# Optimization experiments

Measured on AMD Instinct MI355X. Metric: run time of the kernel, lower is better.

## Reference

```python
import jax, jax.numpy as jnp
import numpy as np


def setup_inputs() -> dict:
    key = jax.random.key(0)
    ks = jax.random.split(key, 5)
    b, n, d = 1, 768, 128
    scale = 1.0 / np.sqrt(d)
    x = jax.random.normal(ks[0], (b, n, d), dtype=jnp.float32)
    W_in = jax.random.normal(ks[1], (d, d), dtype=jnp.float32) * scale
    b_in = jax.random.normal(ks[2], (d,), dtype=jnp.float32) * 0.02
    W_out = jax.random.normal(ks[3], (d, d), dtype=jnp.float32) * scale
    b_out = jax.random.normal(ks[4], (d,), dtype=jnp.float32) * 0.02
    return {"x": x, "W_in": W_in, "b_in": b_in, "W_out": W_out, "b_out": b_out}


def reference(x, W_in, b_in, W_out, b_out):
    # proj_in applied to x (original calls it twice on the same input; identical result)
    left = jnp.einsum('bid,ed->bie', x, W_in) + b_in          # [b, n, d]
    # broadcast outer product: [b, i, 1, d] * [b, 1, j, d] -> [b, i, j, d]
    outer = left[:, :, None, :] * left[:, None, :, :]
    # proj_out over feature dim
    out = jnp.einsum('bijd,ed->bije', outer, W_out) + b_out    # [b, n, n, d]
    return out
```

## Files before the change

kernel.cpp:

```cpp
#include <hip/hip_runtime.h>

#define Nn 768
#define Dd 128
#define LDP 136

typedef __attribute__((ext_vector_type(8))) short bf16x8;
typedef __attribute__((ext_vector_type(4))) float f32x4;
typedef __attribute__((ext_vector_type(4))) int   i32x4;

static __device__ __forceinline__ unsigned short f2bf(float f) {
  unsigned int u = __builtin_bit_cast(unsigned int, f);
  u += 0x7fffu + ((u >> 16) & 1u);
  return (unsigned short)(u >> 16);
}
static __device__ __forceinline__ float bf2f(unsigned short h) {
  unsigned int u = ((unsigned int)h) << 16;
  return __builtin_bit_cast(float, u);
}
static __device__ __forceinline__ unsigned int cvtpk(float lo, float hi) {
  unsigned int r;
  asm("v_cvt_pk_bf16_f32 %0, %1, %2" : "=v"(r) : "v"(lo), "v"(hi));
  return r;
}

__global__ __launch_bounds__(128)
void k_left(const float* __restrict__ x, const float* __restrict__ Win,
            const float* __restrict__ bin, unsigned short* __restrict__ left) {
  __shared__ float sx[Dd];
  const int i = blockIdx.x;
  const int e = threadIdx.x;
  sx[e] = x[i * Dd + e];
  __syncthreads();
  const float4* wrow = (const float4*)(Win + e * Dd);
  float a0 = 0.f, a1 = 0.f, a2 = 0.f, a3 = 0.f;
#pragma unroll
  for (int d4 = 0; d4 < Dd / 4; d4 += 4) {
    float4 w0 = wrow[d4+0], w1 = wrow[d4+1], w2 = wrow[d4+2], w3 = wrow[d4+3];
    a0 += sx[4*d4+ 0]*w0.x + sx[4*d4+ 1]*w0.y + sx[4*d4+ 2]*w0.z + sx[4*d4+ 3]*w0.w;
    a1 += sx[4*d4+ 4]*w1.x + sx[4*d4+ 5]*w1.y + sx[4*d4+ 6]*w1.z + sx[4*d4+ 7]*w1.w;
    a2 += sx[4*d4+ 8]*w2.x + sx[4*d4+ 9]*w2.y + sx[4*d4+10]*w2.z + sx[4*d4+11]*w2.w;
    a3 += sx[4*d4+12]*w3.x + sx[4*d4+13]*w3.y + sx[4*d4+14]*w3.z + sx[4*d4+15]*w3.w;
  }
  left[i * Dd + e] = f2bf(((a0 + a1) + (a2 + a3)) + bin[e]);
}

__global__ __launch_bounds__(256, 3)
void k_outer(const unsigned short* __restrict__ left, const float* __restrict__ Wout,
             const float* __restrict__ bout, float* __restrict__ out) {
  __shared__ __attribute__((aligned(16))) unsigned short sB[128 * LDP];
  __shared__ float sLi[Dd];
  __shared__ float sBo[Dd];

  const int jt = blockIdx.x;
  const int i  = blockIdx.y;
  const int t  = threadIdx.x;

  if (t < Dd) {
    sLi[t] = bf2f(left[i * Dd + t]);
    sBo[t] = bout[t];
  }
  __syncthreads();

  {
    const int row = t >> 4;
    const int c8  = (t & 15) * 8;
    float l[8];
#pragma unroll
    for (int q = 0; q < 8; ++q) l[q] = sLi[c8 + q];
#pragma unroll
    for (int it = 0; it < 8; ++it) {
      const int r = row + it * 16;
      const float4* wp = (const float4*)(Wout + r * Dd + c8);
      float4 w0 = wp[0], w1 = wp[1];
      i32x4 vb;
      vb[0] = (int)cvtpk(w0.x * l[0], w0.y * l[1]);
      vb[1] = (int)cvtpk(w0.z * l[2], w0.w * l[3]);
      vb[2] = (int)cvtpk(w1.x * l[4], w1.y * l[5]);
      vb[3] = (int)cvtpk(w1.z * l[6], w1.w * l[7]);
      *(i32x4*)(sB + r * LDP + c8) = vb;
    }
  }
  __syncthreads();

  const int wid  = t >> 6;
  const int lane = t & 63;
  const int l15  = lane & 15;
  const int kq   = (lane >> 4) * 8;

  const unsigned short* gA = left + (size_t)(jt * 128 + wid * 32 + l15) * Dd;

  f32x4 acc[2][8] = {};
#pragma unroll
  for (int kb = 0; kb < 4; ++kb) {
    const int k = kb * 32 + kq;
    bf16x8 a0 = *(const bf16x8*)(gA + k);
    bf16x8 a1 = *(const bf16x8*)(gA + 16 * Dd + k);
#pragma unroll
    for (int n = 0; n < 8; ++n) {
      bf16x8 b = *(const bf16x8*)(sB + (n * 16 + l15) * LDP + k);
      acc[0][n] = __builtin_amdgcn_mfma_f32_16x16x32_bf16(a0, b, acc[0][n], 0, 0, 0);
      acc[1][n] = __builtin_amdgcn_mfma_f32_16x16x32_bf16(a1, b, acc[1][n], 0, 0, 0);
    }
  }

#pragma unroll
  for (int jb = 0; jb < 2; ++jb) {
#pragma unroll
    for (int r = 0; r < 4; ++r) {
      const int j = jt * 128 + wid * 32 + jb * 16 + (lane >> 4) * 4 + r;
      float* orow = out + ((size_t)i * Nn + j) * Dd;
#pragma unroll
      for (int n = 0; n < 8; ++n) {
        const int e = n * 16 + l15;
        orow[e] = acc[jb][n][r] + sBo[e];
      }
    }
  }
}

extern "C" void kernel_launch(void* const* d_in, const int* in_sizes, int n_in,
                              void* d_out, int out_size, void* d_ws, size_t ws_size,
                              hipStream_t stream) {
  const float* x    = (const float*)d_in[0];
  const float* Win  = (const float*)d_in[1];
  const float* bin  = (const float*)d_in[2];
  const float* Wout = (const float*)d_in[3];
  const float* bout = (const float*)d_in[4];
  float* out = (float*)d_out;
  unsigned short* left = (unsigned short*)d_ws;

  k_left<<<Nn, Dd, 0, stream>>>(x, Win, bin, left);
  dim3 grid(Nn / 128, Nn);
  k_outer<<<grid, 256, 0, stream>>>(left, Wout, bout, out);
}
```

Baseline: 67.06 us.

## Keep scaled Wout fragments in registers and drop LDS staging in outer kernel

The outer-product kernel now builds its B operand (Wout scaled by left[i]) directly into registers per wave, each wave owning 32 output features, instead of staging the whole 128x128 scaled matrix in LDS with two barriers. The A operand (left rows for j) is read from global for all 128 j per wave. The left projection also writes an fp32 copy so B uses the unrounded left[i]. Occupancy hint rises from 3 to 4 blocks. This removes LDS traffic and syncs but makes every wave load all A rows and changes the store pattern to 16-float segments per row.

```diff
diff --git a/kernel.cpp b/kernel.cpp
--- a/kernel.cpp
+++ b/kernel.cpp
@@ -2,7 +2,6 @@
 
 #define Nn 768
 #define Dd 128
-#define LDP 136
 
 typedef __attribute__((ext_vector_type(8))) short bf16x8;
 typedef __attribute__((ext_vector_type(4))) float f32x4;
@@ -13,10 +12,6 @@
   u += 0x7fffu + ((u >> 16) & 1u);
   return (unsigned short)(u >> 16);
 }
-static __device__ __forceinline__ float bf2f(unsigned short h) {
-  unsigned int u = ((unsigned int)h) << 16;
-  return __builtin_bit_cast(float, u);
-}
 static __device__ __forceinline__ unsigned int cvtpk(float lo, float hi) {
   unsigned int r;
   asm("v_cvt_pk_bf16_f32 %0, %1, %2" : "=v"(r) : "v"(lo), "v"(hi));
@@ -25,7 +20,8 @@
 
 __global__ __launch_bounds__(128)
 void k_left(const float* __restrict__ x, const float* __restrict__ Win,
-            const float* __restrict__ bin, unsigned short* __restrict__ left) {
+            const float* __restrict__ bin, unsigned short* __restrict__ left,
+            float* __restrict__ left_f) {
   __shared__ float sx[Dd];
   const int i = blockIdx.x;
   const int e = threadIdx.x;
@@ -41,79 +37,71 @@
     a2 += sx[4*d4+ 8]*w2.x + sx[4*d4+ 9]*w2.y + sx[4*d4+10]*w2.z + sx[4*d4+11]*w2.w;
     a3 += sx[4*d4+12]*w3.x + sx[4*d4+13]*w3.y + sx[4*d4+14]*w3.z + sx[4*d4+15]*w3.w;
   }
-  left[i * Dd + e] = f2bf(((a0 + a1) + (a2 + a3)) + bin[e]);
+  const float v = ((a0 + a1) + (a2 + a3)) + bin[e];
+  left_f[i * Dd + e] = v;
+  left[i * Dd + e]   = f2bf(v);
 }
 
-__global__ __launch_bounds__(256, 3)
-void k_outer(const unsigned short* __restrict__ left, const float* __restrict__ Wout,
+__global__ __launch_bounds__(256, 4)
+void k_outer(const unsigned short* __restrict__ left,
+             const float* __restrict__ left_f,
+             const float* __restrict__ Wout,
              const float* __restrict__ bout, float* __restrict__ out) {
-  __shared__ __attribute__((aligned(16))) unsigned short sB[128 * LDP];
-  __shared__ float sLi[Dd];
-  __shared__ float sBo[Dd];
-
   const int jt = blockIdx.x;
   const int i  = blockIdx.y;
   const int t  = threadIdx.x;
 
-  if (t < Dd) {
-    sLi[t] = bf2f(left[i * Dd + t]);
-    sBo[t] = bout[t];
-  }
-  __syncthreads();
-
-  {
-    const int row = t >> 4;
-    const int c8  = (t & 15) * 8;
-    float l[8];
-#pragma unroll
-    for (int q = 0; q < 8; ++q) l[q] = sLi[c8 + q];
-#pragma unroll
-    for (int it = 0; it < 8; ++it) {
-      const int r = row + it * 16;
-      const float4* wp = (const float4*)(Wout + r * Dd + c8);
-      float4 w0 = wp[0], w1 = wp[1];
-      i32x4 vb;
-      vb[0] = (int)cvtpk(w0.x * l[0], w0.y * l[1]);
-      vb[1] = (int)cvtpk(w0.z * l[2], w0.w * l[3]);
-      vb[2] = (int)cvtpk(w1.x * l[4], w1.y * l[5]);
-      vb[3] = (int)cvtpk(w1.z * l[6], w1.w * l[7]);
-      *(i32x4*)(sB + r * LDP + c8) = vb;
-    }
-  }
-  __syncthreads();
-
   const int wid  = t >> 6;
   const int lane = t & 63;
   const int l15  = lane & 15;
-  const int kq   = (lane >> 4) * 8;
+  const int koct = (lane >> 4) * 8;
 
-  const unsigned short* gA = left + (size_t)(jt * 128 + wid * 32 + l15) * Dd;
-
-  f32x4 acc[2][8] = {};
+  bf16x8 B[2][4];
+  float bias[2];
+  const float* lfi = left_f + i * Dd;
 #pragma unroll
-  for (int kb = 0; kb < 4; ++kb) {
-    const int k = kb * 32 + kq;
-    bf16x8 a0 = *(const bf16x8*)(gA + k);
-    bf16x8 a1 = *(const bf16x8*)(gA + 16 * Dd + k);
+  for (int m = 0; m < 2; ++m) {
+    const int e = wid * 32 + m * 16 + l15;
+    bias[m] = bout[e];
+    const float* wrow = Wout + e * Dd;
 #pragma unroll
-    for (int n = 0; n < 8; ++n) {
-      bf16x8 b = *(const bf16x8*)(sB + (n * 16 + l15) * LDP + k);
-      acc[0][n] = __builtin_amdgcn_mfma_f32_16x16x32_bf16(a0, b, acc[0][n], 0, 0, 0);
-      acc[1][n] = __builtin_amdgcn_mfma_f32_16x16x32_bf16(a1, b, acc[1][n], 0, 0, 0);
+    for (int kb = 0; kb < 4; ++kb) {
+      const int k = kb * 32 + koct;
+      const float4* wp = (const float4*)(wrow + k);
+      const float4* lp = (const float4*)(lfi + k);
+      float4 w0 = wp[0], w1 = wp[1];
+      float4 f0 = lp[0], f1 = lp[1];
+      i32x4 vb;
+      vb[0] = (int)cvtpk(w0.x * f0.x, w0.y * f0.y);
+      vb[1] = (int)cvtpk(w0.z * f0.z, w0.w * f0.w);
+      vb[2] = (int)cvtpk(w1.x * f1.x, w1.y * f1.y);
+      vb[3] = (int)cvtpk(w1.z * f1.z, w1.w * f1.w);
+      B[m][kb] = __builtin_bit_cast(bf16x8, vb);
     }
   }
 
+  f32x4 acc[8][2] = {};
+  const unsigned short* gA0 = left + (size_t)(jt * 128 + l15) * Dd + koct;
 #pragma unroll
-  for (int jb = 0; jb < 2; ++jb) {
+  for (int jf = 0; jf < 8; ++jf) {
+    const unsigned short* gA = gA0 + (size_t)jf * 16 * Dd;
+#pragma unroll
+    for (int kb = 0; kb < 4; ++kb) {
+      bf16x8 a = *(const bf16x8*)(gA + kb * 32);
+      acc[jf][0] = __builtin_amdgcn_mfma_f32_16x16x32_bf16(a, B[0][kb], acc[jf][0], 0, 0, 0);
+      acc[jf][1] = __builtin_amdgcn_mfma_f32_16x16x32_bf16(a, B[1][kb], acc[jf][1], 0, 0, 0);
+    }
+  }
+
+  const int e0 = wid * 32 + l15;
+#pragma unroll
+  for (int jf = 0; jf < 8; ++jf) {
 #pragma unroll
     for (int r = 0; r < 4; ++r) {
-      const int j = jt * 128 + wid * 32 + jb * 16 + (lane >> 4) * 4 + r;
+      const int j = jt * 128 + jf * 16 + (lane >> 4) * 4 + r;
       float* orow = out + ((size_t)i * Nn + j) * Dd;
-#pragma unroll
-      for (int n = 0; n < 8; ++n) {
-        const int e = n * 16 + l15;
-        orow[e] = acc[jb][n][r] + sBo[e];
-      }
+      orow[e0]      = acc[jf][0][r] + bias[0];
+      orow[e0 + 16] = acc[jf][1][r] + bias[1];
     }
   }
 }
@@ -127,9 +115,10 @@
   const float* Wout = (const float*)d_in[3];
   const float* bout = (const float*)d_in[4];
   float* out = (float*)d_out;
-  unsigned short* left = (unsigned short*)d_ws;
+  unsigned short* left  = (unsigned short*)d_ws;
+  float*          left_f = (float*)((char*)d_ws + 256 * 1024);
 
-  k_left<<<Nn, Dd, 0, stream>>>(x, Win, bin, left);
+  k_left<<<Nn, Dd, 0, stream>>>(x, Win, bin, left, left_f);
   dim3 grid(Nn / 128, Nn);
-  k_outer<<<grid, 256, 0, stream>>>(left, Wout, bout, out);
+  k_outer<<<grid, 256, 0, stream>>>(left, left_f, Wout, bout, out);
 }
```

Result: slower. 129.4 us (+92.9%).
